# Performance work log

Measured on AMD Instinct MI355X. Metric: run time of the kernel, lower is better.

The kernel has to match this reference:

```python
import jax, jax.numpy as jnp
import numpy as np

# qshift_a: Kingsbury 10-tap Q-shift filters (sum(h0a) = sqrt(2)).
_H0A = np.array([0.0351638365171441, 0.0, -0.0883294244510729,
                 0.233890320607236, 0.760272369066126, 0.587518297723561,
                 0.0, -0.114301837144249, 0.0, 0.0], dtype=np.float64)
_H0B = _H0A[::-1].copy()
_ALT = (-1.0) ** np.arange(10)
_H1A = _H0B * _ALT            # highpass tree a
_H1B = _H1A[::-1].copy()
# synthesis filters (g0a = h0b, g0b = h0a, g1a = h1b, g1b = h1a)
G0A = _H0B.astype(np.float32)
G0B = _H0A.astype(np.float32)
G1A = _H1B.astype(np.float32)
G1B = _H1A.astype(np.float32)


def _reflect(x, minx, maxx):
    # dtcwt symmetric-extension index reflection (static, numpy)
    x = np.asarray(x, dtype=np.float64)
    rng = maxx - minx
    rng2 = 2.0 * rng
    mod = np.fmod(x - minx, rng2)
    normed = np.where(mod < 0, mod + rng2, mod)
    out = np.where(normed >= rng, rng2 - normed, normed) + minx
    return out.astype(np.int64)


def _colifilt(X, ha, hb):
    # X: (B, C, r, c) -> (B, C, 2r, c). ha, hb are 1-D numpy filters (static).
    m = ha.shape[0]
    m2 = m // 2
    assert m2 % 2 == 1, 'implemented for 10/14/18-tap qshift (m/2 odd)'
    b, ch, r, c = X.shape
    r2 = r // 2
    xe = _reflect(np.arange(-m2, r + m2), -0.5, r - 0.5)   # static indices
    t = np.arange(2, r + m - 1, 2)
    if float(np.sum(ha * hb)) > 0:
        ta, tb = t, t - 1
    else:
        ta, tb = t - 1, t
    Xa = X[:, :, xe[ta], :]   # (B, C, r/2 + m/2 - 1, c)
    Xb = X[:, :, xe[tb], :]
    hao, hae = ha[0::2], ha[1::2]
    hbo, hbe = hb[0::2], hb[1::2]

    def vconv(Z, h):
        # valid convolution along dim 2 (true conv: filter flipped)
        hf = h[::-1]
        out = Z[:, :, 0:r2, :] * float(hf[0])
        for k in range(1, m2):
            out = out + Z[:, :, k:k + r2, :] * float(hf[k])
        return out

    y = jnp.stack([vconv(Xb, hao), vconv(Xa, hbo),
                   vconv(Xb, hae), vconv(Xa, hbe)], axis=3)  # (B,C,r/2,4,c)
    return y.reshape(b, ch, 2 * r, c)


def _rowifilt(X, ha, hb):
    return jnp.swapaxes(_colifilt(jnp.swapaxes(X, 2, 3), ha, hb), 2, 3)


def _c2q(wr, wi):
    # complex pair of subbands -> real quad image. wr, wi: (B, C, 2, H, W) -> (B, C, 2H, 2W)
    w1r, w2r = wr[:, :, 0], wr[:, :, 1]
    w1i, w2i = wi[:, :, 0], wi[:, :, 1]
    x1 = w1r + w2r
    x2 = w1i + w2i
    x3 = w1i - w2i
    x4 = w2r - w1r
    b, c, h, w = x1.shape
    top = jnp.stack([x1, x2], axis=-1).reshape(b, c, h, 2 * w)
    bot = jnp.stack([x3, x4], axis=-1).reshape(b, c, h, 2 * w)
    y = jnp.stack([top, bot], axis=-2).reshape(b, c, 2 * h, 2 * w)
    return y * np.float32(1.0 / np.sqrt(2.0))


def setup_inputs() -> dict:
    key = jax.random.key(0)
    k1, k2, k3 = jax.random.split(key, 3)
    B, C, H, W = 8, 64, 128, 128
    Yl = jax.random.normal(k1, (B, C, H, W), dtype=jnp.float32)
    Yhr = jax.random.normal(k2, (B, C, 6, H // 2, W // 2), dtype=jnp.float32)
    Yhi = jax.random.normal(k3, (B, C, 6, H // 2, W // 2), dtype=jnp.float32)
    return {"Yl": Yl, "Yhr": Yhr, "Yhi": Yhi}


def reference(Yl, Yhr, Yhi):
    lh = _c2q(Yhr[:, :, 0:6:5], Yhi[:, :, 0:6:5])
    hl = _c2q(Yhr[:, :, 2:4:1], Yhi[:, :, 2:4:1])
    hh = _c2q(Yhr[:, :, 1:5:3], Yhi[:, :, 1:5:3])
    y1 = _rowifilt(Yl, G0B, G0A) + _rowifilt(hl, G1B, G1A)
    y2 = _rowifilt(lh, G0B, G0A) + _rowifilt(hh, G1B, G1A)
    return _colifilt(y1, G0B, G0A) + _colifilt(y2, G1B, G1A)
```

## Files before the change

kernel.cpp:

```cpp
#include <hip/hip_runtime.h>
#include <hip/hip_bf16.h>

#define NTHREADS 256

__device__ __forceinline__ int reflect128(int p) {
    p = (p < 0) ? (-p - 1) : p;
    p = (p >= 128) ? (255 - p) : p;
    return p;
}
__device__ __forceinline__ int reflect64(int p) {
    p = (p < 0) ? (-p - 1) : p;
    p = (p >= 64) ? (127 - p) : p;
    return p;
}

__constant__ int   cs0[4] = {2, 1, 1, 0};
__constant__ int   cs1[4] = {1, 2, 0, 1};
__constant__ float cc0[4][3] = {
    { 0.760272369066126f, -0.0883294244510729f,  0.0351638365171441f},
    { 0.233890320607236f,  0.587518297723561f,  -0.114301837144249f},
    {-0.114301837144249f,  0.587518297723561f,   0.233890320607236f},
    { 0.0351638365171441f, -0.0883294244510729f, 0.760272369066126f}};
__constant__ float cc1[4][3] = {
    { 0.233890320607236f,  0.587518297723561f,  -0.114301837144249f},
    {-0.760272369066126f,  0.0883294244510729f, -0.0351638365171441f},
    {-0.0351638365171441f, 0.0883294244510729f, -0.760272369066126f},
    {-0.114301837144249f,  0.587518297723561f,   0.233890320607236f}};

__global__ __launch_bounds__(NTHREADS, 4)
void dtcwt_inv_kernel(const float* __restrict__ Yl,
                      const float* __restrict__ Yhr,
                      const float* __restrict__ Yhi,
                      float* __restrict__ out)
{
    const int tid   = threadIdx.x;
    const int ct    = blockIdx.x;
    const int rt    = blockIdx.y;
    const int plane = blockIdx.z;

    const int OR0 = rt * 64, OC0 = ct * 64;
    const int i0r = OR0 >> 2, i0c = OC0 >> 2;
    const int yrb = 2 * i0r - 4;
    const int icb = 2 * i0c - 4;

    const float* yl = Yl + (size_t)plane * (128 * 128);
    const float* hr = Yhr + (size_t)plane * 6 * 4096;
    const float* hi = Yhi + (size_t)plane * 6 * 4096;

    __shared__ float sYl[2][40][20];
    __shared__ float sLh[2][40][20];
    __shared__ float sHl[2][40][20];
    __shared__ float sHh[2][40][20];
    __shared__ __hip_bfloat16 sY1[2][20][64];
    __shared__ __hip_bfloat16 sY2[2][20][64];

    const float RS2 = 0.70710678118654752440f;

    for (int e = tid; e < 1600; e += NTHREADS) {
        const int t = e / 40;
        const int u = e - t * 40;
        const int ry = reflect128(yrb + t);
        const int ic = reflect128(icb + u);
        sYl[u & 1][t][u >> 1] = yl[ry * 128 + ic];
    }

    for (int e = tid; e < 400; e += NTHREADS) {
        const int t2 = e / 20;
        const int u2 = e - t2 * 20;
        const int r2 = reflect64(i0r - 2 + t2);
        const int c2 = reflect64(i0c - 2 + u2);
        const int off = r2 * 64 + c2;
        float ar0 = hr[0 * 4096 + off], ar1 = hr[1 * 4096 + off], ar2 = hr[2 * 4096 + off];
        float ar3 = hr[3 * 4096 + off], ar4 = hr[4 * 4096 + off], ar5 = hr[5 * 4096 + off];
        float ai0 = hi[0 * 4096 + off], ai1 = hi[1 * 4096 + off], ai2 = hi[2 * 4096 + off];
        float ai3 = hi[3 * 4096 + off], ai4 = hi[4 * 4096 + off], ai5 = hi[5 * 4096 + off];
#pragma unroll
        for (int dt = 0; dt < 2; ++dt) {
#pragma unroll
            for (int du = 0; du < 2; ++du) {
                const int t = 2 * t2 + dt, u = 2 * u2 + du;
                const int p = reflect128(yrb + t) & 1;
                const int q = reflect128(icb + u) & 1;
                const float sA = (p & q) ? -RS2 : RS2;
                const float sB = (p & ~q & 1) ? -RS2 : RS2;
                float b0, b5, b2v, b3, b1, b4;
                if (p == q) { b0 = ar0; b5 = ar5; b2v = ar2; b3 = ar3; b1 = ar1; b4 = ar4; }
                else        { b0 = ai0; b5 = ai5; b2v = ai2; b3 = ai3; b1 = ai1; b4 = ai4; }
                sLh[du][t][u2] = sA * b0 + sB * b5;
                sHl[du][t][u2] = sA * b2v + sB * b3;
                sHh[du][t][u2] = sA * b1 + sB * b4;
            }
        }
    }
    __syncthreads();

    const int c  = tid & 63;
    const int jc = c & 3;
    const int pc0 = jc & 1;
    const int pc1 = pc0 ^ 1;
    const int h0 = (c >> 2) + cs0[jc];
    const int h1 = (c >> 2) + cs1[jc];
    const float a0 = cc0[jc][0], a1 = cc0[jc][1], a2 = cc0[jc][2];
    const float b0w = cc1[jc][0], b1w = cc1[jc][1], b2w = cc1[jc][2];

    for (int t = tid >> 6; t < 40; t += 4) {
        const float* yl0 = &sYl[pc0][t][h0];
        const float* hl1 = &sHl[pc1][t][h1];
        const float* lh0 = &sLh[pc0][t][h0];
        const float* hh1 = &sHh[pc1][t][h1];
        float acc1 = yl0[0] * a0 + yl0[1] * a1 + yl0[2] * a2
                   + hl1[0] * b0w + hl1[1] * b1w + hl1[2] * b2w;
        float acc2 = lh0[0] * a0 + lh0[1] * a1 + lh0[2] * a2
                   + hh1[0] * b0w + hh1[1] * b1w + hh1[2] * b2w;
        sY1[t & 1][t >> 1][c] = __float2bfloat16(acc1);
        sY2[t & 1][t >> 1][c] = __float2bfloat16(acc2);
    }
    __syncthreads();

    const int j  = tid >> 6;
    const int p0 = j & 1, p1 = p0 ^ 1;
    const int g0 = cs0[j], g1 = cs1[j];
    const float d0 = cc0[j][0], d1 = cc0[j][1], d2 = cc0[j][2];
    const float e0 = cc1[j][0], e1 = cc1[j][1], e2 = cc1[j][2];

    float* orow = out + ((size_t)plane * 256 + OR0 + j) * 256 + OC0 + c;
#pragma unroll
    for (int m = 0; m < 16; ++m) {
        float acc = __bfloat162float(sY1[p0][m + g0][c]) * d0
                  + __bfloat162float(sY1[p0][m + g0 + 1][c]) * d1
                  + __bfloat162float(sY1[p0][m + g0 + 2][c]) * d2
                  + __bfloat162float(sY2[p1][m + g1][c]) * e0
                  + __bfloat162float(sY2[p1][m + g1 + 1][c]) * e1
                  + __bfloat162float(sY2[p1][m + g1 + 2][c]) * e2;
        orow[(size_t)(4 * m) * 256] = acc;
    }
}

extern "C" void kernel_launch(void* const* d_in, const int* in_sizes, int n_in,
                              void* d_out, int out_size, void* d_ws, size_t ws_size,
                              hipStream_t stream) {
    const float* Yl  = (const float*)d_in[0];
    const float* Yhr = (const float*)d_in[1];
    const float* Yhi = (const float*)d_in[2];
    float* out = (float*)d_out;

    const int planes = in_sizes[0] / (128 * 128);
    dim3 grid(4, 4, planes);
    dtcwt_inv_kernel<<<grid, NTHREADS, 0, stream>>>(Yl, Yhr, Yhi, out);
}
```

Measured before the change: 276.8 us.

## Read Yl directly from global in row pass and drop its shared staging

Removes the shared-memory staging of the Yl tile. The row filter pass now reads Yl straight from global memory, using reflected row and column indices precomputed per thread, which drops one shared-store loop. The highpass shared arrays change from parity-split to plain layouts, the c2q reflection-parity logic is simplified, and launch bounds rise to allow more resident blocks. The cost is more global loads in the row pass, which rely on L1/L2 caching, and possible shared bank conflicts from the new stride-2 shared access pattern.

```diff
diff --git a/kernel.cpp b/kernel.cpp
--- a/kernel.cpp
+++ b/kernel.cpp
@@ -6,11 +6,6 @@
 __device__ __forceinline__ int reflect128(int p) {
     p = (p < 0) ? (-p - 1) : p;
     p = (p >= 128) ? (255 - p) : p;
-    return p;
-}
-__device__ __forceinline__ int reflect64(int p) {
-    p = (p < 0) ? (-p - 1) : p;
-    p = (p >= 64) ? (127 - p) : p;
     return p;
 }
 
@@ -27,7 +22,7 @@
     {-0.0351638365171441f, 0.0883294244510729f, -0.760272369066126f},
     {-0.114301837144249f,  0.587518297723561f,   0.233890320607236f}};
 
-__global__ __launch_bounds__(NTHREADS, 4)
+__global__ __launch_bounds__(NTHREADS, 5)
 void dtcwt_inv_kernel(const float* __restrict__ Yl,
                       const float* __restrict__ Yhr,
                       const float* __restrict__ Yhi,
@@ -47,48 +42,43 @@
     const float* hr = Yhr + (size_t)plane * 6 * 4096;
     const float* hi = Yhi + (size_t)plane * 6 * 4096;
 
-    __shared__ float sYl[2][40][20];
-    __shared__ float sLh[2][40][20];
-    __shared__ float sHl[2][40][20];
-    __shared__ float sHh[2][40][20];
-    __shared__ __hip_bfloat16 sY1[2][20][64];
-    __shared__ __hip_bfloat16 sY2[2][20][64];
+    __shared__ float sLh[40][40];
+    __shared__ float sHl[40][40];
+    __shared__ float sHh[40][40];
+    __shared__ __hip_bfloat16 sY1[40][64];
+    __shared__ __hip_bfloat16 sY2[40][64];
 
     const float RS2 = 0.70710678118654752440f;
-
-    for (int e = tid; e < 1600; e += NTHREADS) {
-        const int t = e / 40;
-        const int u = e - t * 40;
-        const int ry = reflect128(yrb + t);
-        const int ic = reflect128(icb + u);
-        sYl[u & 1][t][u >> 1] = yl[ry * 128 + ic];
-    }
 
     for (int e = tid; e < 400; e += NTHREADS) {
         const int t2 = e / 20;
         const int u2 = e - t2 * 20;
-        const int r2 = reflect64(i0r - 2 + t2);
-        const int c2 = reflect64(i0c - 2 + u2);
+        const int ar = i0r - 2 + t2;
+        const int ac = i0c - 2 + u2;
+        const int oobr = (ar < 0) | (ar >= 64);
+        const int oobc = (ac < 0) | (ac >= 64);
+        const int r2 = oobr ? ((ar < 0) ? (-ar - 1) : (127 - ar)) : ar;
+        const int c2 = oobc ? ((ac < 0) ? (-ac - 1) : (127 - ac)) : ac;
         const int off = r2 * 64 + c2;
-        float ar0 = hr[0 * 4096 + off], ar1 = hr[1 * 4096 + off], ar2 = hr[2 * 4096 + off];
-        float ar3 = hr[3 * 4096 + off], ar4 = hr[4 * 4096 + off], ar5 = hr[5 * 4096 + off];
-        float ai0 = hi[0 * 4096 + off], ai1 = hi[1 * 4096 + off], ai2 = hi[2 * 4096 + off];
-        float ai3 = hi[3 * 4096 + off], ai4 = hi[4 * 4096 + off], ai5 = hi[5 * 4096 + off];
+        const float ar0 = hr[off], ar1 = hr[4096 + off], ar2 = hr[2 * 4096 + off];
+        const float ar3 = hr[3 * 4096 + off], ar4 = hr[4 * 4096 + off], ar5 = hr[5 * 4096 + off];
+        const float ai0 = hi[off], ai1 = hi[4096 + off], ai2 = hi[2 * 4096 + off];
+        const float ai3 = hi[3 * 4096 + off], ai4 = hi[4 * 4096 + off], ai5 = hi[5 * 4096 + off];
 #pragma unroll
         for (int dt = 0; dt < 2; ++dt) {
 #pragma unroll
             for (int du = 0; du < 2; ++du) {
-                const int t = 2 * t2 + dt, u = 2 * u2 + du;
-                const int p = reflect128(yrb + t) & 1;
-                const int q = reflect128(icb + u) & 1;
+                const int p = dt ^ oobr;
+                const int q = du ^ oobc;
                 const float sA = (p & q) ? -RS2 : RS2;
-                const float sB = (p & ~q & 1) ? -RS2 : RS2;
+                const float sB = (p & (q ^ 1)) ? -RS2 : RS2;
                 float b0, b5, b2v, b3, b1, b4;
                 if (p == q) { b0 = ar0; b5 = ar5; b2v = ar2; b3 = ar3; b1 = ar1; b4 = ar4; }
                 else        { b0 = ai0; b5 = ai5; b2v = ai2; b3 = ai3; b1 = ai1; b4 = ai4; }
-                sLh[du][t][u2] = sA * b0 + sB * b5;
-                sHl[du][t][u2] = sA * b2v + sB * b3;
-                sHh[du][t][u2] = sA * b1 + sB * b4;
+                const int t = 2 * t2 + dt, u = 2 * u2 + du;
+                sLh[t][u] = sA * b0 + sB * b5;
+                sHl[t][u] = sA * b2v + sB * b3;
+                sHh[t][u] = sA * b1 + sB * b4;
             }
         }
     }
@@ -96,43 +86,44 @@
 
     const int c  = tid & 63;
     const int jc = c & 3;
-    const int pc0 = jc & 1;
-    const int pc1 = pc0 ^ 1;
-    const int h0 = (c >> 2) + cs0[jc];
-    const int h1 = (c >> 2) + cs1[jc];
+    const int q2 = c >> 2;
     const float a0 = cc0[jc][0], a1 = cc0[jc][1], a2 = cc0[jc][2];
     const float b0w = cc1[jc][0], b1w = cc1[jc][1], b2w = cc1[jc][2];
+    const int ub0 = 2 * q2 + (jc & 1) + 2 * cs0[jc];
+    const int ub1 = 2 * q2 + ((jc & 1) ^ 1) + 2 * cs1[jc];
+    const int ic0 = reflect128(icb + ub0);
+    const int ic1 = reflect128(icb + ub0 + 2);
+    const int ic2 = reflect128(icb + ub0 + 4);
 
     for (int t = tid >> 6; t < 40; t += 4) {
-        const float* yl0 = &sYl[pc0][t][h0];
-        const float* hl1 = &sHl[pc1][t][h1];
-        const float* lh0 = &sLh[pc0][t][h0];
-        const float* hh1 = &sHh[pc1][t][h1];
-        float acc1 = yl0[0] * a0 + yl0[1] * a1 + yl0[2] * a2
-                   + hl1[0] * b0w + hl1[1] * b1w + hl1[2] * b2w;
-        float acc2 = lh0[0] * a0 + lh0[1] * a1 + lh0[2] * a2
-                   + hh1[0] * b0w + hh1[1] * b1w + hh1[2] * b2w;
-        sY1[t & 1][t >> 1][c] = __float2bfloat16(acc1);
-        sY2[t & 1][t >> 1][c] = __float2bfloat16(acc2);
+        const int ry = reflect128(yrb + t);
+        const float* yrow = yl + ry * 128;
+        float acc1 = yrow[ic0] * a0 + yrow[ic1] * a1 + yrow[ic2] * a2
+                   + sHl[t][ub1] * b0w + sHl[t][ub1 + 2] * b1w + sHl[t][ub1 + 4] * b2w;
+        float acc2 = sLh[t][ub0] * a0 + sLh[t][ub0 + 2] * a1 + sLh[t][ub0 + 4] * a2
+                   + sHh[t][ub1] * b0w + sHh[t][ub1 + 2] * b1w + sHh[t][ub1 + 4] * b2w;
+        sY1[t][c] = __float2bfloat16(acc1);
+        sY2[t][c] = __float2bfloat16(acc2);
     }
     __syncthreads();
 
     const int j  = tid >> 6;
     const int p0 = j & 1, p1 = p0 ^ 1;
-    const int g0 = cs0[j], g1 = cs1[j];
+    const int r0 = p0 + 2 * cs0[j];
+    const int r1 = p1 + 2 * cs1[j];
     const float d0 = cc0[j][0], d1 = cc0[j][1], d2 = cc0[j][2];
     const float e0 = cc1[j][0], e1 = cc1[j][1], e2 = cc1[j][2];
 
-    float* orow = out + ((size_t)plane * 256 + OR0 + j) * 256 + OC0 + c;
+    float* op = out + ((size_t)plane * 256 + OR0 + j) * 256 + OC0 + c;
 #pragma unroll
     for (int m = 0; m < 16; ++m) {
-        float acc = __bfloat162float(sY1[p0][m + g0][c]) * d0
-                  + __bfloat162float(sY1[p0][m + g0 + 1][c]) * d1
-                  + __bfloat162float(sY1[p0][m + g0 + 2][c]) * d2
-                  + __bfloat162float(sY2[p1][m + g1][c]) * e0
-                  + __bfloat162float(sY2[p1][m + g1 + 1][c]) * e1
-                  + __bfloat162float(sY2[p1][m + g1 + 2][c]) * e2;
-        orow[(size_t)(4 * m) * 256] = acc;
+        float acc = __bfloat162float(sY1[2 * m + r0][c]) * d0
+                  + __bfloat162float(sY1[2 * m + r0 + 2][c]) * d1
+                  + __bfloat162float(sY1[2 * m + r0 + 4][c]) * d2
+                  + __bfloat162float(sY2[2 * m + r1][c]) * e0
+                  + __bfloat162float(sY2[2 * m + r1 + 2][c]) * e1
+                  + __bfloat162float(sY2[2 * m + r1 + 4][c]) * e2;
+        op[(size_t)m * 1024] = acc;
     }
 }
 
```

New measurement: 274.9 us. About the same (-0.7%).
